# Performance work log

Measured on AMD Instinct MI355X. Metric: run time of the kernel, lower is better.

Reference implementation:

```python
import jax, jax.numpy as jnp
import numpy as np

B, G, C, Hmlp, R = 4, 2048, 384, 1536, 96
NH = 6          # attention heads
V = 6           # number of 2D views (len(out_transform_2d))
NC = 1024       # number of clusters for segment_csr
GX = GY = 32    # grid shape per view
SCALE_FACTOR = 0.5  # args.scale_factor
COEF_PRO = 0.5      # args.coef_pro
EPS_LN = 1e-5
EPS_BN = 1e-5


def _forward(x, center1, norm1_g, norm1_b, qkv_w, proj_w, proj_b, norm2_g, norm2_b,
             fc1_w, fc1_b, fc2_w, fc2_b, ada1_w, ada1_b, ada2_w, ada2_b,
             bn3_g, bn3_b, bn3_m, bn3_v, bn2_g, bn2_b, bn2_m, bn2_v,
             norm3_g, norm3_b, a1_qkv_w, a1_proj_w, a1_proj_b,
             mask, idx_ptr, sorted_cluster_indices, cluster, flat_grid_index,
             grid_shape_x, grid_shape_y):
    B_, G1, C_ = x.shape
    hd = C_ // NH

    def ln(t, g, b):
        mu = t.mean(-1, keepdims=True)
        var = ((t - mu) ** 2).mean(-1, keepdims=True)
        return (t - mu) * jax.lax.rsqrt(var + EPS_LN) * g + b

    def bn_gelu(t, g, b, m, v):  # BatchNorm1d (eval) + GELU
        t = (t - m) * jax.lax.rsqrt(v + EPS_BN) * g + b
        return jax.nn.gelu(t, approximate=False)

    # ---- multi-head self-attention sublayer ----
    h = ln(x, norm1_g, norm1_b)
    qkv = (h @ qkv_w).reshape(B_, G1, 3, NH, hd).transpose(2, 0, 3, 1, 4)
    q, k, v = qkv[0], qkv[1], qkv[2]
    attn = jax.nn.softmax(jnp.einsum('bhqd,bhkd->bhqk', q, k) * hd ** -0.5, axis=-1)
    o = jnp.einsum('bhqk,bhkd->bhqd', attn, v).transpose(0, 2, 1, 3).reshape(B_, G1, C_)
    x = x + o @ proj_w + proj_b

    # ---- MLP + adapter sublayer ----
    h2 = ln(x, norm2_g, norm2_b)
    ffn = jax.nn.gelu(h2 @ fc1_w + fc1_b, approximate=False) @ fc2_w + fc2_b
    a = ffn @ ada1_w + ada1_b
    a = a * jax.nn.sigmoid(1.702 * a)      # QuickGELU
    ada = a @ ada2_w + ada2_b
    x = x + ffn + SCALE_FACTOR * ada

    cls_x = x[:, :1]
    pts = x[:, 1:]
    Gp = G1 - 1
    N = B_ * Gp

    # ---- 3D branch: segment_csr max/mean over clusters, gather back ----
    feat = pts.reshape(N, C_)
    fs = feat[sorted_cluster_indices]
    seg = cluster[sorted_cluster_indices]          # sorted segment ids (CSR order)
    nc = idx_ptr.shape[0] - 1
    cnt = jax.ops.segment_sum(jnp.ones((N,), feat.dtype), seg, nc)
    fsum = jax.ops.segment_sum(fs, seg, nc)
    fmax = jax.ops.segment_max(fs, seg, nc)
    fmax = jnp.where(cnt[:, None] > 0, fmax, 0.0)
    fmean = fsum / jnp.maximum(cnt, 1.0)[:, None]
    x3d = bn_gelu(fmax + fmean, bn3_g, bn3_b, bn3_m, bn3_v)[cluster].reshape(pts.shape)

    # ---- per-view 2D branch: masked attn + scatter_max/mean over grid cells ----
    dim_size = center1.shape[0] * grid_shape_x * grid_shape_y
    nviews = center1.shape[1]
    views = []
    for i in range(nviews):
        fx = pts.reshape(N, C_)
        h3 = ln(fx, norm3_g[i], norm3_b[i]).reshape(B_, Gp, C_)
        qkv1 = (h3 @ a1_qkv_w[i]).reshape(B_, Gp, 3, C_).transpose(2, 0, 1, 3)
        q1, k1, v1 = qkv1[0], qkv1[1], qkv1[2]
        s = jnp.einsum('bqd,bkd->bqk', q1, k1) * C_ ** -0.5
        s = jnp.where(mask[i][None], s, jnp.finfo(s.dtype).min)
        o1 = jnp.einsum('bqk,bkd->bqd', jax.nn.softmax(s, axis=-1), v1) @ a1_proj_w[i] + a1_proj_b[i]
        fx = o1.reshape(N, C_) + fx
        gi = flat_grid_index[i]
        gc = jax.ops.segment_sum(jnp.ones((N,), fx.dtype), gi, dim_size)
        gs = jax.ops.segment_sum(fx, gi, dim_size)
        gm = jax.ops.segment_max(fx, gi, dim_size)
        gm = jnp.where(gc[:, None] > 0, gm, 0.0)
        cell = bn_gelu(gs / jnp.maximum(gc, 1.0)[:, None] + gm,
                       bn2_g[i], bn2_b[i], bn2_m[i], bn2_v[i])
        views.append(cell[gi].reshape(pts.shape))

    # ---- cosine-similarity weighted fusion across views ----
    x_sup = jnp.stack(views, 0)                     # [V,B,G,C]
    dot = jnp.sum(x_sup * x3d[None], -1)
    nrm = jnp.linalg.norm(x_sup, axis=-1) * jnp.linalg.norm(x3d, axis=-1)[None]
    sims = (dot / jnp.maximum(nrm, 1e-8) + 1.0) / 2.0
    sims = sims / sims.sum(0, keepdims=True)
    x_sup_w = jnp.sum(x_sup * sims[..., None], 0)
    pts = pts + COEF_PRO * x_sup_w
    return jnp.concatenate([cls_x, pts], axis=1)


def setup_inputs() -> dict:
    rng = np.random.default_rng(0)
    key = jax.random.key(0)
    N = B * G
    # consistent cluster structure: every cluster non-empty
    cluster = np.concatenate([np.arange(NC), rng.integers(0, NC, N - NC)]).astype(np.int32)
    rng.shuffle(cluster)
    sorted_idx = np.argsort(cluster, kind='stable').astype(np.int32)
    counts = np.bincount(cluster, minlength=NC)
    idx_ptr = np.concatenate([[0], np.cumsum(counts)]).astype(np.int32)
    flat_grid_index = rng.integers(0, B * GX * GY, (V, N)).astype(np.int32)
    mask = (rng.random((V, G, G)) < 0.25) | np.eye(G, dtype=bool)[None]
    ks = jax.random.split(key, 16)
    f32 = jnp.float32
    def w(k, shape, s=0.02):
        return jax.random.normal(k, shape, f32) * s
    return {
        'x': jax.random.normal(ks[0], (B, G + 1, C), f32),
        'center1': jax.random.normal(ks[1], (B, V, G, 3), f32),
        'norm1_g': jnp.ones((C,), f32), 'norm1_b': jnp.zeros((C,), f32),
        'qkv_w': w(ks[2], (C, 3 * C)), 'proj_w': w(ks[3], (C, C)), 'proj_b': jnp.zeros((C,), f32),
        'norm2_g': jnp.ones((C,), f32), 'norm2_b': jnp.zeros((C,), f32),
        'fc1_w': w(ks[4], (C, Hmlp)), 'fc1_b': jnp.zeros((Hmlp,), f32),
        'fc2_w': w(ks[5], (Hmlp, C)), 'fc2_b': jnp.zeros((C,), f32),
        'ada1_w': w(ks[6], (C, R)), 'ada1_b': jnp.zeros((R,), f32),
        'ada2_w': w(ks[7], (R, C)), 'ada2_b': jnp.zeros((C,), f32),
        'bn3_g': jnp.ones((C,), f32), 'bn3_b': jnp.zeros((C,), f32),
        'bn3_m': w(ks[8], (C,), 0.1), 'bn3_v': jnp.ones((C,), f32) + jax.random.uniform(ks[9], (C,), f32) * 0.5,
        'bn2_g': jnp.ones((V, C), f32), 'bn2_b': jnp.zeros((V, C), f32),
        'bn2_m': w(ks[10], (V, C), 0.1), 'bn2_v': jnp.ones((V, C), f32) + jax.random.uniform(ks[11], (V, C), f32) * 0.5,
        'norm3_g': jnp.ones((V, C), f32), 'norm3_b': jnp.zeros((V, C), f32),
        'a1_qkv_w': w(ks[12], (V, C, 3 * C)), 'a1_proj_w': w(ks[13], (V, C, C)), 'a1_proj_b': jnp.zeros((V, C), f32),
        'mask': jnp.asarray(mask),
        'idx_ptr': jnp.asarray(idx_ptr),
        'sorted_cluster_indices': jnp.asarray(sorted_idx),
        'cluster': jnp.asarray(cluster),
        'flat_grid_index': jnp.asarray(flat_grid_index),
        'grid_shape_x': GX,
        'grid_shape_y': GY,
    }


def reference(x, center1, norm1_g, norm1_b, qkv_w, proj_w, proj_b, norm2_g, norm2_b,
              fc1_w, fc1_b, fc2_w, fc2_b, ada1_w, ada1_b, ada2_w, ada2_b,
              bn3_g, bn3_b, bn3_m, bn3_v, bn2_g, bn2_b, bn2_m, bn2_v,
              norm3_g, norm3_b, a1_qkv_w, a1_proj_w, a1_proj_b,
              mask, idx_ptr, sorted_cluster_indices, cluster, flat_grid_index,
              grid_shape_x, grid_shape_y):
    return _forward(x, center1, norm1_g, norm1_b, qkv_w, proj_w, proj_b, norm2_g, norm2_b,
                    fc1_w, fc1_b, fc2_w, fc2_b, ada1_w, ada1_b, ada2_w, ada2_b,
                    bn3_g, bn3_b, bn3_m, bn3_v, bn2_g, bn2_b, bn2_m, bn2_v,
                    norm3_g, norm3_b, a1_qkv_w, a1_proj_w, a1_proj_b,
                    mask, idx_ptr, sorted_cluster_indices, cluster, flat_grid_index,
                    grid_shape_x, grid_shape_y)
```

## Files before the change

kernel.cpp:

```cpp
#include <hip/hip_runtime.h>
#include <math.h>

typedef short bf16x8 __attribute__((ext_vector_type(8)));
typedef float f32x4 __attribute__((ext_vector_type(4)));

#define GLL16(g, l) \
  __builtin_amdgcn_global_load_lds((__attribute__((address_space(1))) const unsigned int*)(g), \
                                   (__attribute__((address_space(3))) unsigned int*)(l), 16, 0, 0)

__device__ __forceinline__ float wsum(float v){
  #pragma unroll
  for (int o=32;o;o>>=1) v += __shfl_xor(v,o);
  return v;
}
__device__ __forceinline__ float geluf(float x){
  return 0.5f*x*(1.0f+erff(x*0.7071067811865475f));
}
__device__ __forceinline__ short fbf(float f){
  unsigned u = __float_as_uint(f);
  unsigned r = (u + 0x7fffu + ((u>>16)&1u)) >> 16;
  return (short)r;
}
__device__ __forceinline__ float bff(short s){
  return __uint_as_float(((unsigned)(unsigned short)s)<<16);
}
__device__ __forceinline__ unsigned fkey(float f){
  unsigned b=__float_as_uint(f);
  return (b&0x80000000u)? ~b : (b|0x80000000u);
}
__device__ __forceinline__ float fdec(unsigned k){
  unsigned b=(k&0x80000000u)? (k&0x7fffffffu) : ~k;
  return __uint_as_float(b);
}

__global__ void detect_mask_kernel(const int* __restrict__ m, long long n, int* flag){
  long long i = (long long)blockIdx.x*256 + threadIdx.x;
  bool bad = (i<n) && (m[i]!=0 && m[i]!=1);
  if (__any(bad)) { if ((threadIdx.x&63)==0) atomicOr(flag,1); }
}
__global__ void mask_bits_kernel(const void* __restrict__ m, unsigned long long* __restrict__ mb,
                                 long long nOut, const int* __restrict__ flag){
  long long i = (long long)blockIdx.x*256 + threadIdx.x;
  if (i>=nOut) return;
  int mode = *flag;
  unsigned long long bits = 0;
  if (mode){
    const unsigned long long* p = (const unsigned long long*)((const unsigned char*)m + i*64);
    #pragma unroll
    for (int k=0;k<8;k++){
      unsigned long long v = p[k];
      #pragma unroll
      for (int b=0;b<8;b++)
        bits |= (unsigned long long)(((v>>(b*8))&0xffull)!=0) << (k*8+b);
    }
  } else {
    const int4* p = (const int4*)((const int*)m + i*64);
    #pragma unroll
    for (int k=0;k<16;k++){
      int4 v = p[k];
      bits |= (unsigned long long)(v.x!=0) << (k*4+0);
      bits |= (unsigned long long)(v.y!=0) << (k*4+1);
      bits |= (unsigned long long)(v.z!=0) << (k*4+2);
      bits |= (unsigned long long)(v.w!=0) << (k*4+3);
    }
  }
  mb[i] = bits;
}

__device__ __forceinline__ float epi(float v, const float* bias, int col, int act){
  if (bias) v += bias[col];
  if (act==1) v = geluf(v);
  else if (act==2) v = v*(1.f/(1.f+__expf(-1.702f*v)));
  return v;
}

#define XBM 128
#define XBN 128
#define XBK 32
__global__ __launch_bounds__(256)
void gemm_bf16_big(const short* __restrict__ A, int lda, long long sA,
                   const short* __restrict__ B, int ldb, long long sB,
                   const float* __restrict__ bias, long long sBias,
                   const float* __restrict__ res, int ldr, long long sR,
                   void* __restrict__ out, int ldo, long long sO, int outbf16,
                   int M, int N, int K, int act, int KS)
{
  __shared__ short As[XBM*XBK];
  __shared__ short Bs[XBN*XBK];
  int zz = blockIdx.z;
  int z = zz / KS, ks = zz - z*KS;
  A += (long long)z*sA; B += (long long)z*sB;
  if (res) res += (long long)z*sR;
  if (bias) bias += (long long)z*sBias;
  float* outF = (float*)out + (long long)z*sO;
  short* outH = (short*)out + (long long)z*sO;

  int tid = threadIdx.x;
  int rowBase = blockIdx.y*XBM;
  int colBase = blockIdx.x*XBN;

  int Kc = ((K + KS*XBK - 1)/(KS*XBK))*XBK;
  int kbeg = ks*Kc;
  int kend = min(K, kbeg+Kc);
  if (kbeg >= kend) return;

  int w = tid>>6;
  int lane = tid&63;
  int lm = lane&15, quad = lane>>4;
  int waveM = w>>1, waveN = w&1;

  int arow0 = min(rowBase + w*32 + lm,      M-1);
  int arow1 = min(rowBase + w*32 + 16 + lm, M-1);
  int brow0 = min(colBase + w*32 + lm,      N-1);
  int brow1 = min(colBase + w*32 + 16 + lm, N-1);
  const short* Ag0 = A + (long long)arow0*lda + quad*8;
  const short* Ag1 = A + (long long)arow1*lda + quad*8;
  const short* Bg0 = B + (long long)brow0*ldb + quad*8;
  const short* Bg1 = B + (long long)brow1*ldb + quad*8;
  short* Al0 = &As[(w*2+0)*512];
  short* Al1 = &As[(w*2+1)*512];
  short* Bl0 = &Bs[(w*2+0)*512];
  short* Bl1 = &Bs[(w*2+1)*512];

  f32x4 acc[4][4] = {};

  for (int k0=kbeg; k0<kend; k0+=XBK){
    GLL16(Ag0 + k0, Al0);
    GLL16(Ag1 + k0, Al1);
    GLL16(Bg0 + k0, Bl0);
    GLL16(Bg1 + k0, Bl1);
    __syncthreads();
    bf16x8 af[4], bfr[4];
    #pragma unroll
    for (int tm=0;tm<4;tm++) af[tm]  = *(bf16x8*)&As[(waveM*4+tm)*512 + quad*128 + lm*8];
    #pragma unroll
    for (int tn=0;tn<4;tn++) bfr[tn] = *(bf16x8*)&Bs[(waveN*4+tn)*512 + quad*128 + lm*8];
    #pragma unroll
    for (int tm=0;tm<4;tm++)
      #pragma unroll
      for (int tn=0;tn<4;tn++)
        acc[tm][tn] = __builtin_amdgcn_mfma_f32_16x16x32_bf16(af[tm], bfr[tn], acc[tm][tn], 0,0,0);
    __syncthreads();
  }

  #pragma unroll
  for (int tm=0;tm<4;tm++){
    #pragma unroll
    for (int tn=0;tn<4;tn++){
      int col = colBase + waveN*64 + tn*16 + lm;
      if (col>=N) continue;
      #pragma unroll
      for (int reg=0;reg<4;reg++){
        int row = rowBase + waveM*64 + tm*16 + quad*4 + reg;
        if (row>=M) continue;
        float v = acc[tm][tn][reg];
        if (KS>1){ atomicAdd(&outF[(long long)row*ldo+col], v); continue; }
        v = epi(v, bias, col, act);
        if (res) v += res[(long long)row*ldr+col];
        if (outbf16) outH[(long long)row*ldo+col] = fbf(v);
        else         outF[(long long)row*ldo+col] = v;
      }
    }
  }
}

__global__ __launch_bounds__(256)
void gemm_bf16_s(const short* __restrict__ A, int lda, long long sA,
                 const short* __restrict__ B, int ldb, long long sB,
                 const float* __restrict__ bias, long long sBias,
                 const float* __restrict__ res, int ldr, long long sR,
                 void* __restrict__ out, int ldo, long long sO, int outbf16,
                 int M, int N, int K, int act)
{
  __shared__ short As[64*32];
  __shared__ short Bs[64*32];
  int z = blockIdx.z;
  A += (long long)z*sA; B += (long long)z*sB;
  if (res) res += (long long)z*sR;
  if (bias) bias += (long long)z*sBias;
  float* outF = (float*)out + (long long)z*sO;
  short* outH = (short*)out + (long long)z*sO;

  int tid = threadIdx.x;
  int rowBase = blockIdx.y*64;
  int colBase = blockIdx.x*64;

  int w = tid>>6;
  int lane = tid&63;
  int lm = lane&15, quad = lane>>4;
  int wm = w>>1, wn = w&1;

  int arow = min(rowBase + w*16 + lm, M-1);
  int brow = min(colBase + w*16 + lm, N-1);
  const short* Ag = A + (long long)arow*lda + quad*8;
  const short* Bg = B + (long long)brow*ldb + quad*8;
  short* Al = &As[w*512];
  short* Bl = &Bs[w*512];

  f32x4 acc[2][2] = {};

  for (int k0=0; k0<K; k0+=32){
    GLL16(Ag + k0, Al);
    GLL16(Bg + k0, Bl);
    __syncthreads();
    bf16x8 af[2], bfr[2];
    #pragma unroll
    for (int tm=0;tm<2;tm++) af[tm]  = *(bf16x8*)&As[(wm*2+tm)*512 + quad*128 + lm*8];
    #pragma unroll
    for (int tn=0;tn<2;tn++) bfr[tn] = *(bf16x8*)&Bs[(wn*2+tn)*512 + quad*128 + lm*8];
    #pragma unroll
    for (int tm=0;tm<2;tm++)
      #pragma unroll
      for (int tn=0;tn<2;tn++)
        acc[tm][tn] = __builtin_amdgcn_mfma_f32_16x16x32_bf16(af[tm], bfr[tn], acc[tm][tn], 0,0,0);
    __syncthreads();
  }

  #pragma unroll
  for (int tm=0;tm<2;tm++){
    #pragma unroll
    for (int tn=0;tn<2;tn++){
      int col = colBase + wn*32 + tn*16 + lm;
      if (col>=N) continue;
      #pragma unroll
      for (int reg=0;reg<4;reg++){
        int row = rowBase + wm*32 + tm*16 + quad*4 + reg;
        if (row>=M) continue;
        float v = epi(acc[tm][tn][reg], bias, col, act);
        if (res) v += res[(long long)row*ldr+col];
        if (outbf16==2){
          int bb = row>>11;
          outH[((long long)bb*384 + col)*2048 + (row&2047)] = fbf(v);
        }
        else if (outbf16) outH[(long long)row*ldo+col] = fbf(v);
        else              outF[(long long)row*ldo+col] = v;
      }
    }
  }
}

__global__ __launch_bounds__(256,2)
void flash_view(const short* __restrict__ QK6, const short* __restrict__ Vt6,
                const unsigned long long* __restrict__ maskbits, short* __restrict__ O6)
{
  __shared__ char lds[58112];
  const float scale = 0.05103103630798288f;
  int id = blockIdx.x;
  int xcd = id & 7;
  int j = id >> 3;
  int vb = xcd*3 + (j>>5);
  int qt = j & 31;
  int v = vb >> 2, b = vb & 3;
  int tid=threadIdx.x, w=tid>>6, lane=tid&63, lm=lane&15, quad=lane>>4;

  const short* Qp = QK6 + ((long long)v*8192 + b*2048 + qt*64)*768;
  const short* Kp = QK6 + ((long long)v*8192 + b*2048)*768 + 384;
  const short* Vp = Vt6 + (long long)(v*4+b)*384*2048;
  const unsigned long long* Mb = maskbits + (long long)v*2048*32 + (long long)qt*64*32;
  short* Op = O6 + ((long long)v*8192 + b*2048 + qt*64)*384;

  short* P = (short*)(lds + 49152);
  float* alphaL = (float*)(lds + 57856);

  bf16x8 af[12];
  #pragma unroll
  for (int c=0;c<12;c++)
    af[c] = *(const bf16x8*)(Qp + (long long)(w*16+lm)*768 + c*32 + quad*8);

  float m_i[4], l_i[4];
  #pragma unroll
  for (int r=0;r<4;r++){ m_i[r]=-3.0e38f; l_i[r]=0.f; }
  f32x4 Oacc[4][6] = {};

  for (int kt=0; kt<32; kt++){
    #pragma unroll
    for (int c=0;c<12;c++)
      GLL16(Kp + (long long)(kt*64 + w*16 + lm)*768 + c*32 + quad*8, (short*)(lds + w*12288 + c*1024));
    __syncthreads();
    unsigned long long mb[4];
    #pragma unroll
    for (int r=0;r<4;r++)
      mb[r] = Mb[(long long)(w*16+quad*4+r)*32 + kt];
    f32x4 S[4];
    #pragma unroll
    for (int i=0;i<4;i++) S[i] = (f32x4){0.f,0.f,0.f,0.f};
    __builtin_amdgcn_s_setprio(1);
    #pragma unroll
    for (int kc=0;kc<12;kc++){
      #pragma unroll
      for (int ct=0;ct<4;ct++){
        bf16x8 bf = *(bf16x8*)(lds + ct*12288 + kc*1024 + quad*256 + lm*16);
        S[ct] = __builtin_amdgcn_mfma_f32_16x16x32_bf16(af[kc], bf, S[ct], 0,0,0);
      }
    }
    __builtin_amdgcn_s_setprio(0);
    #pragma unroll
    for (int r=0;r<4;r++){
      unsigned long long t = mb[r] >> lm;
      S[0][r] = ((unsigned)t      & 1u) ? S[0][r]*scale : -3.0e38f;
      S[1][r] = ((unsigned)(t>>16)& 1u) ? S[1][r]*scale : -3.0e38f;
      S[2][r] = ((unsigned)(t>>32)& 1u) ? S[2][r]*scale : -3.0e38f;
      S[3][r] = ((unsigned)(t>>48)& 1u) ? S[3][r]*scale : -3.0e38f;
    }
    float alpha[4], mnew[4];
    #pragma unroll
    for (int r=0;r<4;r++){
      float rm = S[0][r];
      #pragma unroll
      for (int ct=1;ct<4;ct++) rm = fmaxf(rm, S[ct][r]);
      #pragma unroll
      for (int o=1;o<16;o<<=1) rm = fmaxf(rm, __shfl_xor(rm, o));
      mnew[r] = fmaxf(m_i[r], rm);
      alpha[r] = __expf(m_i[r]-mnew[r]);
      m_i[r] = mnew[r];
    }
    float rs[4] = {0.f,0.f,0.f,0.f};
    #pragma unroll
    for (int ct=0;ct<4;ct++){
      #pragma unroll
      for (int r=0;r<4;r++){
        float sv = S[ct][r];
        float p = (sv > -1.0e37f) ? __expf(sv - mnew[r]) : 0.f;
        rs[r] += p;
        P[(w*16+quad*4+r)*68 + ct*16 + lm] = fbf(p);
      }
    }
    #pragma unroll
    for (int r=0;r<4;r++){
      #pragma unroll
      for (int o=1;o<16;o<<=1) rs[r] += __shfl_xor(rs[r], o);
      l_i[r] = l_i[r]*alpha[r] + rs[r];
    }
    if (lm==0){
      #pragma unroll
      for (int r=0;r<4;r++) alphaL[w*16+quad*4+r] = alpha[r];
    }
    bf16x8 Vreg[6][2];
    #pragma unroll
    for (int jj=0;jj<6;jj++)
      #pragma unroll
      for (int kk=0;kk<2;kk++)
        Vreg[jj][kk] = *(const bf16x8*)(Vp + (long long)((w*6+jj)*16+lm)*2048 + kt*64 + kk*32 + quad*8);
    __syncthreads();
    f32x4 am[4];
    #pragma unroll
    for (int m=0;m<4;m++) am[m] = *(f32x4*)&alphaL[m*16 + quad*4];
    #pragma unroll
    for (int m=0;m<4;m++)
      #pragma unroll
      for (int tn=0;tn<6;tn++)
        Oacc[m][tn] *= am[m];
    __builtin_amdgcn_s_setprio(1);
    #pragma unroll
    for (int kk=0;kk<2;kk++){
      bf16x8 ap[4];
      #pragma unroll
      for (int m=0;m<4;m++) ap[m] = *(bf16x8*)&P[(m*16+lm)*68 + kk*32 + quad*8];
      #pragma unroll
      for (int tn=0;tn<6;tn++){
        #pragma unroll
        for (int m=0;m<4;m++)
          Oacc[m][tn] = __builtin_amdgcn_mfma_f32_16x16x32_bf16(ap[m], Vreg[tn][kk], Oacc[m][tn], 0,0,0);
      }
    }
    __builtin_amdgcn_s_setprio(0);
  }

  __syncthreads();
  if (lm==0){
    #pragma unroll
    for (int r=0;r<4;r++) alphaL[w*16+quad*4+r] = l_i[r];
  }
  __syncthreads();
  f32x4 lv[4];
  #pragma unroll
  for (int m=0;m<4;m++) lv[m] = *(f32x4*)&alphaL[m*16 + quad*4];
  #pragma unroll
  for (int m=0;m<4;m++){
    #pragma unroll
    for (int tn=0;tn<6;tn++){
      #pragma unroll
      for (int reg=0;reg<4;reg++){
        Op[(long long)(m*16+quad*4+reg)*384 + (w*6+tn)*16 + lm] = fbf(Oacc[m][tn][reg] / lv[m][reg]);
      }
    }
  }
}

__global__ __launch_bounds__(256,4)
void flash_inner(const short* __restrict__ QKV, const short* __restrict__ Vt,
                 short* __restrict__ O)
{
  __shared__ char lds[17152];
  int id = blockIdx.x;
  int xcd = id & 7;
  int j = id >> 3;
  int bh = xcd*3 + j/33;
  int qt = j%33;
  int b=bh/6, h=bh-b*6;
  int tid=threadIdx.x, w=tid>>6, lane=tid&63, lm=lane&15, quad=lane>>4;

  const short* Qb = QKV + (long long)b*2049*1152 + h*64;
  const short* Kb = Qb + 384;
  const short* Vtp = Vt + (long long)bh*64*2112;
  short* Op = O + ((long long)b*2049 + qt*64)*384 + h*64;

  short* P = (short*)(lds + 8192);
  float* alphaL = (float*)(lds + 16896);

  int qr = min(qt*64 + w*16 + lm, 2048);
  bf16x8 af[2];
  #pragma unroll
  for (int c=0;c<2;c++)
    af[c] = *(const bf16x8*)(Qb + (long long)qr*1152 + c*32 + quad*8);

  float m_i[4], l_i[4];
  #pragma unroll
  for (int r=0;r<4;r++){ m_i[r]=-3.0e38f; l_i[r]=0.f; }
  f32x4 Oacc[4] = {};

  {
    int kr0 = min(w*16 + lm, 2048);
    #pragma unroll
    for (int c=0;c<2;c++)
      GLL16(Kb + (long long)kr0*1152 + c*32 + quad*8, (short*)(lds + w*2048 + c*1024));
  }

  for (int kt=0; kt<33; kt++){
    __syncthreads();
    f32x4 S[4];
    #pragma unroll
    for (int i=0;i<4;i++) S[i] = (f32x4){0.f,0.f,0.f,0.f};
    __builtin_amdgcn_s_setprio(1);
    #pragma unroll
    for (int kc=0;kc<2;kc++){
      #pragma unroll
      for (int ct=0;ct<4;ct++){
        bf16x8 bf = *(bf16x8*)(lds + ct*2048 + kc*1024 + quad*256 + lm*16);
        S[ct] = __builtin_amdgcn_mfma_f32_16x16x32_bf16(af[kc], bf, S[ct], 0,0,0);
      }
    }
    __builtin_amdgcn_s_setprio(0);
    #pragma unroll
    for (int ct=0;ct<4;ct++){
      int scol = kt*64 + ct*16 + lm;
      bool ok = scol <= 2048;
      #pragma unroll
      for (int r=0;r<4;r++) S[ct][r] = ok ? S[ct][r]*0.125f : -3.0e38f;
    }
    float alpha[4], mnew[4];
    #pragma unroll
    for (int r=0;r<4;r++){
      float rm = S[0][r];
      #pragma unroll
      for (int ct=1;ct<4;ct++) rm = fmaxf(rm, S[ct][r]);
      #pragma unroll
      for (int o=1;o<16;o<<=1) rm = fmaxf(rm, __shfl_xor(rm, o));
      mnew[r] = fmaxf(m_i[r], rm);
      alpha[r] = __expf(m_i[r]-mnew[r]);
      m_i[r] = mnew[r];
    }
    float rs[4] = {0.f,0.f,0.f,0.f};
    #pragma unroll
    for (int ct=0;ct<4;ct++){
      #pragma unroll
      for (int r=0;r<4;r++){
        float sv = S[ct][r];
        float p = (sv > -1.0e37f) ? __expf(sv - mnew[r]) : 0.f;
        rs[r] += p;
        P[(w*16+quad*4+r)*68 + ct*16 + lm] = fbf(p);
      }
    }
    #pragma unroll
    for (int r=0;r<4;r++){
      #pragma unroll
      for (int o=1;o<16;o<<=1) rs[r] += __shfl_xor(rs[r], o);
      l_i[r] = l_i[r]*alpha[r] + rs[r];
    }
    if (lm==0){
      #pragma unroll
      for (int r=0;r<4;r++) alphaL[w*16+quad*4+r] = alpha[r];
    }
    bf16x8 Vreg[2];
    #pragma unroll
    for (int kk=0;kk<2;kk++)
      Vreg[kk] = *(const bf16x8*)(Vtp + (long long)(w*16+lm)*2112 + kt*64 + kk*32 + quad*8);
    __syncthreads();
    if (kt < 32){
      int krn = min((kt+1)*64 + w*16 + lm, 2048);
      #pragma unroll
      for (int c=0;c<2;c++)
        GLL16(Kb + (long long)krn*1152 + c*32 + quad*8, (short*)(lds + w*2048 + c*1024));
    }
    f32x4 am[4];
    #pragma unroll
    for (int m=0;m<4;m++) am[m] = *(f32x4*)&alphaL[m*16 + quad*4];
    #pragma unroll
    for (int m=0;m<4;m++) Oacc[m] *= am[m];
    __builtin_amdgcn_s_setprio(1);
    #pragma unroll
    for (int kk=0;kk<2;kk++){
      bf16x8 ap[4];
      #pragma unroll
      for (int m=0;m<4;m++) ap[m] = *(bf16x8*)&P[(m*16+lm)*68 + kk*32 + quad*8];
      #pragma unroll
      for (int m=0;m<4;m++)
        Oacc[m] = __builtin_amdgcn_mfma_f32_16x16x32_bf16(ap[m], Vreg[kk], Oacc[m], 0,0,0);
    }
    __builtin_amdgcn_s_setprio(0);
  }

  __syncthreads();
  if (lm==0){
    #pragma unroll
    for (int r=0;r<4;r++) alphaL[w*16+quad*4+r] = l_i[r];
  }
  __syncthreads();
  f32x4 lv[4];
  #pragma unroll
  for (int m=0;m<4;m++) lv[m] = *(f32x4*)&alphaL[m*16 + quad*4];
  #pragma unroll
  for (int m=0;m<4;m++){
    #pragma unroll
    for (int reg=0;reg<4;reg++){
      int row = qt*64 + m*16 + quad*4 + reg;
      if (row < 2049)
        Op[(long long)(m*16+quad*4+reg)*384 + w*16 + lm] = fbf(Oacc[m][reg] / lv[m][reg]);
    }
  }
}

__global__ __launch_bounds__(128)
void ln_bf16_kernel(const float* __restrict__ in, const float* __restrict__ g,
                    const float* __restrict__ bt, short* __restrict__ out)
{
  long long row = blockIdx.x;
  const float* p = in + row*384;
  int tid = threadIdx.x;
  float v0=p[tid], v1=p[tid+128], v2=p[tid+256];
  float s = v0+v1+v2;
  float ss = v0*v0+v1*v1+v2*v2;
  __shared__ float r1[2], r2[2];
  s = wsum(s); ss = wsum(ss);
  int wid=tid>>6, lane=tid&63;
  if (lane==0){ r1[wid]=s; r2[wid]=ss; }
  __syncthreads();
  float mean=(r1[0]+r1[1])*(1.f/384.f);
  float var =(r2[0]+r2[1])*(1.f/384.f)-mean*mean;
  float rstd=rsqrtf(var+1e-5f);
  short* o = out + row*384;
  o[tid]     = fbf((v0-mean)*rstd*g[tid]+bt[tid]);
  o[tid+128] = fbf((v1-mean)*rstd*g[tid+128]+bt[tid+128]);
  o[tid+256] = fbf((v2-mean)*rstd*g[tid+256]+bt[tid+256]);
}

__global__ __launch_bounds__(128)
void ln6_kernel(const float* __restrict__ in, const float* __restrict__ g6,
                const float* __restrict__ b6, short* __restrict__ out6)
{
  long long row = blockIdx.x;
  const float* p = in + row*384;
  int tid = threadIdx.x;
  float v0=p[tid], v1=p[tid+128], v2=p[tid+256];
  float s = v0+v1+v2;
  float ss = v0*v0+v1*v1+v2*v2;
  __shared__ float r1[2], r2[2];
  s = wsum(s); ss = wsum(ss);
  int wid=tid>>6, lane=tid&63;
  if (lane==0){ r1[wid]=s; r2[wid]=ss; }
  __syncthreads();
  float mean=(r1[0]+r1[1])*(1.f/384.f);
  float var =(r2[0]+r2[1])*(1.f/384.f)-mean*mean;
  float rstd=rsqrtf(var+1e-5f);
  float n0=(v0-mean)*rstd, n1=(v1-mean)*rstd, n2=(v2-mean)*rstd;
  #pragma unroll
  for (int i=0;i<6;i++){
    const float* g = g6 + i*384;
    const float* bt = b6 + i*384;
    short* o = out6 + (long long)i*8192*384 + row*384;
    o[tid]     = fbf(n0*g[tid]+bt[tid]);
    o[tid+128] = fbf(n1*g[tid+128]+bt[tid+128]);
    o[tid+256] = fbf(n2*g[tid+256]+bt[tid+256]);
  }
}

__global__ void cvt_kernel(const float* __restrict__ in, short* __restrict__ out, long long n4){
  long long i = (long long)blockIdx.x*256 + threadIdx.x;
  if (i<n4){
    float4 f = ((const float4*)in)[i];
    short4 s;
    s.x=fbf(f.x); s.y=fbf(f.y); s.z=fbf(f.z); s.w=fbf(f.w);
    ((short4*)out)[i]=s;
  }
}

__global__ __launch_bounds__(256)
void tconv_kernel(const float* __restrict__ in, int ldin, long long sIn, long long sIn2, int zmod,
                  int R, int C, short* __restrict__ out, int ldout, long long sOut)
{
  __shared__ float tile[32][33];
  int z = blockIdx.z;
  const float* ip = in + (long long)(z/zmod)*sIn + (long long)(z%zmod)*sIn2;
  short* op = out + (long long)z*sOut;
  int r0 = blockIdx.x*32;
  int c0 = blockIdx.y*32;
  int tx = threadIdx.x&31, ty = threadIdx.x>>5;
  #pragma unroll
  for (int i=0;i<4;i++){
    int r = r0 + ty + i*8, c = c0 + tx;
    tile[ty+i*8][tx] = (r<R && c<C) ? ip[(long long)r*ldin + c] : 0.f;
  }
  __syncthreads();
  #pragma unroll
  for (int i=0;i<4;i++){
    int oc = c0 + ty + i*8;
    int orr = r0 + tx;
    if (oc<C && orr<ldout) op[(long long)oc*ldout + orr] = fbf(tile[tx][ty+i*8]);
  }
}

__global__ __launch_bounds__(256)
void tconv16_kernel(const short* __restrict__ in, int ldin, long long sIn, long long sIn2, int zmod,
                    int R, int C, short* __restrict__ out, int ldout, long long sOut)
{
  __shared__ short tile[32][34];
  int z = blockIdx.z;
  const short* ip = in + (long long)(z/zmod)*sIn + (long long)(z%zmod)*sIn2;
  short* op = out + (long long)z*sOut;
  int r0 = blockIdx.x*32;
  int c0 = blockIdx.y*32;
  int tx = threadIdx.x&31, ty = threadIdx.x>>5;
  #pragma unroll
  for (int i=0;i<4;i++){
    int r = r0 + ty + i*8, c = c0 + tx;
    tile[ty+i*8][tx] = (r<R && c<C) ? ip[(long long)r*ldin + c] : (short)0;
  }
  __syncthreads();
  #pragma unroll
  for (int i=0;i<4;i++){
    int oc = c0 + ty + i*8;
    int orr = r0 + tx;
    if (oc<C && orr<ldout) op[(long long)oc*ldout + orr] = tile[tx][ty+i*8];
  }
}

__global__ void ew_x2_kernel(float* x1, const float* ffn, const float* ada, long long n){
  long long i=(long long)blockIdx.x*256+threadIdx.x;
  if (i<n) x1[i] = x1[i] + ffn[i] + 0.5f*ada[i];
}
__global__ void copy_pts_kernel(const float* __restrict__ x2, float* __restrict__ pts){
  long long i=(long long)blockIdx.x*256+threadIdx.x;
  if (i < 8192ll*384){
    long long b = i/(2048ll*384);
    long long rem = i%(2048ll*384);
    pts[i] = x2[(b*2049+1)*384 + rem];
  }
}
__global__ void copy_cls_kernel(const float* __restrict__ x2, float* __restrict__ out){
  int i = blockIdx.x*256+threadIdx.x;
  if (i < 4*384){
    int b=i/384, c=i%384;
    out[(long long)b*2049*384 + c] = x2[(long long)b*2049*384 + c];
  }
}

__global__ __launch_bounds__(128)
void scatter_seg_kernel(const float* __restrict__ feat, const int* __restrict__ seg,
                        float* __restrict__ fsum, unsigned* __restrict__ fmax,
                        float* __restrict__ cnt,
                        long long zFeat, long long zSeg, long long zSum, long long zCnt)
{
  int n = blockIdx.x, z = blockIdx.y;
  feat += (long long)z*zFeat; seg += (long long)z*zSeg;
  fsum += (long long)z*zSum; fmax += (long long)z*zSum; cnt += (long long)z*zCnt;
  int s = seg[n];
  const float* p = feat + (long long)n*384;
  int tid = threadIdx.x;
  #pragma unroll
  for (int k=0;k<3;k++){
    int c = tid + k*128;
    float v = p[c];
    atomicAdd(&fsum[(long long)s*384+c], v);
    atomicMax(&fmax[(long long)s*384+c], fkey(v));
  }
  if (tid==0) atomicAdd(&cnt[s], 1.0f);
}

__global__ __launch_bounds__(128)
void cell_kernel(const float* __restrict__ fsum, const unsigned* __restrict__ fmax,
                 const float* __restrict__ cnt,
                 const float* __restrict__ g, const float* __restrict__ bb,
                 const float* __restrict__ m, const float* __restrict__ v,
                 float* __restrict__ out, long long zSum, long long zCnt, long long zP)
{
  int s = blockIdx.x, z = blockIdx.y;
  fsum += (long long)z*zSum; fmax += (long long)z*zSum; cnt += (long long)z*zCnt;
  g += (long long)z*zP; bb += (long long)z*zP; m += (long long)z*zP; v += (long long)z*zP;
  out += (long long)z*zSum;
  float cn = cnt[s];
  float denom = fmaxf(cn, 1.f);
  int tid = threadIdx.x;
  #pragma unroll
  for (int k=0;k<3;k++){
    int c = tid + k*128;
    float mx = (cn>0.f) ? fdec(fmax[(long long)s*384+c]) : 0.f;
    float t = mx + fsum[(long long)s*384+c]/denom;
    t = (t - m[c])*rsqrtf(v[c]+1e-5f)*g[c] + bb[c];
    out[(long long)s*384+c] = geluf(t);
  }
}

__global__ __launch_bounds__(128)
void combine_kernel(const float* __restrict__ pts, const float* __restrict__ cell3,
                    const int* __restrict__ cluster, const float* __restrict__ cell2,
                    const int* __restrict__ gidx, float* __restrict__ out)
{
  int n = blockIdx.x;
  int tid = threadIdx.x;
  __shared__ float sdot[6], ssq[6], sw[6];
  __shared__ int soff[6];
  __shared__ float red[2][2];
  __shared__ float sn3;
  const float* x3 = cell3 + (long long)cluster[n]*384;
  int wid=tid>>6, lane=tid&63;
  float sq=0.f;
  for (int c=tid;c<384;c+=128){ float v=x3[c]; sq+=v*v; }
  sq = wsum(sq);
  if (lane==0) red[0][wid]=sq;
  __syncthreads();
  if (tid==0) sn3 = sqrtf(red[0][0]+red[0][1]);
  __syncthreads();
  for (int i=0;i<6;i++){
    int gi = gidx[(long long)i*8192 + n];
    if (tid==0) soff[i]=gi;
    const float* r = cell2 + ((long long)i*4096 + gi)*384;
    float d=0.f, s2=0.f;
    for (int c=tid;c<384;c+=128){ float a=r[c]; d+=a*x3[c]; s2+=a*a; }
    d = wsum(d); s2 = wsum(s2);
    if (lane==0){ red[0][wid]=d; red[1][wid]=s2; }
    __syncthreads();
    if (tid==0){ sdot[i]=red[0][0]+red[0][1]; ssq[i]=red[1][0]+red[1][1]; }
    __syncthreads();
  }
  if (tid==0){
    float ssumv=0.f; float sims[6];
    for (int i=0;i<6;i++){
      float nrm = sqrtf(ssq[i])*sn3;
      float s = (sdot[i]/fmaxf(nrm,1e-8f) + 1.f)*0.5f;
      sims[i]=s; ssumv+=s;
    }
    for (int i=0;i<6;i++) sw[i]=sims[i]/ssumv;
  }
  __syncthreads();
  int b = n>>11, gp = n&2047;
  float* o = out + ((long long)(b*2049 + 1 + gp))*384;
  for (int c=tid;c<384;c+=128){
    float acc=0.f;
    #pragma unroll
    for (int i=0;i<6;i++){
      const float* r = cell2 + ((long long)i*4096 + soff[i])*384;
      acc += sw[i]*r[c];
    }
    o[c] = pts[(long long)n*384+c] + 0.5f*acc;
  }
}

static inline void launch_gemm16b(hipStream_t s, const short* A,int lda,long long sA,
  const short* B,int ldb,long long sB, const float* bias, long long sBias,
  const float* res,int ldr,long long sR, void* out,int ldo,long long sO,int outbf16,
  int M,int N,int K,int act,int nz,int KS)
{
  dim3 g((N+XBN-1)/XBN,(M+XBM-1)/XBM,(unsigned)(nz*KS));
  hipLaunchKernelGGL(gemm_bf16_big,g,dim3(256),0,s,
    A,lda,sA,B,ldb,sB,bias,sBias,res,ldr,sR,out,ldo,sO,outbf16,M,N,K,act,KS);
}
static inline void launch_gemm16s(hipStream_t s, const short* A,int lda,long long sA,
  const short* B,int ldb,long long sB, const float* bias, long long sBias,
  const float* res,int ldr,long long sR, void* out,int ldo,long long sO,int outbf16,
  int M,int N,int K,int act,int nz)
{
  dim3 g((N+63)/64,(M+63)/64,(unsigned)nz);
  hipLaunchKernelGGL(gemm_bf16_s,g,dim3(256),0,s,
    A,lda,sA,B,ldb,sB,bias,sBias,res,ldr,sR,out,ldo,sO,outbf16,M,N,K,act);
}
static inline void launch_tconv(hipStream_t s, const float* in,int ldin,long long sIn,long long sIn2,int zmod,
  int R,int C, short* out,int ldout,long long sOut,int nz)
{
  dim3 g((ldout+31)/32,(C+31)/32,(unsigned)nz);
  hipLaunchKernelGGL(tconv_kernel,g,dim3(256),0,s, in,ldin,sIn,sIn2,zmod,R,C,out,ldout,sOut);
}
static inline void launch_tconv16(hipStream_t s, const short* in,int ldin,long long sIn,long long sIn2,int zmod,
  int R,int C, short* out,int ldout,long long sOut,int nz)
{
  dim3 g((ldout+31)/32,(C+31)/32,(unsigned)nz);
  hipLaunchKernelGGL(tconv16_kernel,g,dim3(256),0,s, in,ldin,sIn,sIn2,zmod,R,C,out,ldout,sOut);
}
static inline void launch_cvt(hipStream_t s, const float* in, short* out, long long n){
  long long n4 = n/4;
  hipLaunchKernelGGL(cvt_kernel,dim3((unsigned)((n4+255)/256)),dim3(256),0,s,in,out,n4);
}

extern "C" void kernel_launch(void* const* d_in, const int* in_sizes, int n_in,
                              void* d_out, int out_size, void* d_ws, size_t ws_size,
                              hipStream_t stream)
{
  const float* x       = (const float*)d_in[0];
  const float* norm1_g = (const float*)d_in[2];
  const float* norm1_b = (const float*)d_in[3];
  const float* qkv_w   = (const float*)d_in[4];
  const float* proj_w  = (const float*)d_in[5];
  const float* proj_b  = (const float*)d_in[6];
  const float* norm2_g = (const float*)d_in[7];
  const float* norm2_b = (const float*)d_in[8];
  const float* fc1_w   = (const float*)d_in[9];
  const float* fc1_b   = (const float*)d_in[10];
  const float* fc2_w   = (const float*)d_in[11];
  const float* fc2_b   = (const float*)d_in[12];
  const float* ada1_w  = (const float*)d_in[13];
  const float* ada1_b  = (const float*)d_in[14];
  const float* ada2_w  = (const float*)d_in[15];
  const float* ada2_b  = (const float*)d_in[16];
  const float* bn3_g   = (const float*)d_in[17];
  const float* bn3_b   = (const float*)d_in[18];
  const float* bn3_m   = (const float*)d_in[19];
  const float* bn3_v   = (const float*)d_in[20];
  const float* bn2_g   = (const float*)d_in[21];
  const float* bn2_b   = (const float*)d_in[22];
  const float* bn2_m   = (const float*)d_in[23];
  const float* bn2_v   = (const float*)d_in[24];
  const float* norm3_g = (const float*)d_in[25];
  const float* norm3_b = (const float*)d_in[26];
  const float* a1_qkv_w  = (const float*)d_in[27];
  const float* a1_proj_w = (const float*)d_in[28];
  const float* a1_proj_b = (const float*)d_in[29];
  const void*  maskp     = d_in[30];
  const int*   cluster   = (const int*)d_in[33];
  const int*   fgi       = (const int*)d_in[34];
  float* out = (float*)d_out;

  size_t off = 0;
  char* wsb = (char*)d_ws;
  auto alloc = [&](size_t bytes)->void*{
    void* p = wsb + off;
    off += (bytes + 255) & ~(size_t)255;
    return p;
  };
  short*    bufHh = (short*)alloc(8196ll*384*2);
  float*    ptsb  = (float*)alloc(8192ll*384*4);
  float*    cnt   = (float*)alloc(1024*4);
  float*    fsum  = (float*)alloc(1024ll*384*4);
  unsigned* fmaxe = (unsigned*)alloc(1024ll*384*4);
  float*    cell3 = (float*)alloc(1024ll*384*4);
  unsigned char* maskb = (unsigned char*)alloc(6ll*2048*2048);
  float*    gc6   = (float*)alloc(6ll*4096*4);
  short*    qkvT  = (short*)alloc(1152ll*384*2);
  short*    projT = (short*)alloc(384ll*384*2);
  short*    fc1T  = (short*)alloc(1536ll*384*2);
  short*    fc2T  = (short*)alloc(384ll*1536*2);
  short*    ada1T = (short*)alloc(96ll*384*2);
  short*    ada2T = (short*)alloc(384ll*96*2);
  short*    a1qkvT  = (short*)alloc(6ll*1152*384*2);
  short*    a1projT = (short*)alloc(6ll*384*384*2);
  int*      flag  = (int*)alloc(256);
  char* arena = (char*)alloc(188743680);
  char* A0 = arena;
  char* A1 = arena + 75497472;
  char* A2 = arena + 150994944;
  short* bufQh = (short*)(A0 + 0);
  float* bufO  = (float*)(A0 + 20971520);
  short* bufOh = (short*)(A0 + 35651584);
  short* bufAh = (short*)(A0 + 44040192);
  float* bufX  = (float*)(A0 + 46137344);
  float* bufAda= (float*)(A0 + 0);
  short* Vt_i  = (short*)(A1 + 0);
  short* bufTh = (short*)(A1 + 8388608);
  short* QK6   = (short*)(A0 + 0);
  short* Vt6   = (short*)(A1 + 0);
  short* O6    = (short*)(A2 + 0);
  short* bufHh6= (short*)(A2 + 0);
  float* bufT6 = (float*)(A0 + 0);
  float* gsum6 = (float*)(A1 + 0);
  unsigned* gmaxe6 = (unsigned*)(A1 + 37748736);
  float* cell2 = (float*)(A0 + 0);

  unsigned long long* maskbits = (unsigned long long*)maskb;

  hipMemsetAsync(flag, 0, 4, stream);
  {
    long long nInt = 6ll*2048*2048/4;
    detect_mask_kernel<<<dim3((unsigned)((nInt+255)/256)),dim3(256),0,stream>>>((const int*)maskp, nInt, flag);
    long long nOut = 6ll*2048*32;
    mask_bits_kernel<<<dim3((unsigned)((nOut+255)/256)),dim3(256),0,stream>>>(maskp, maskbits, nOut, flag);
  }

  launch_tconv(stream, qkv_w, 1152, 0,0,1, 384,1152, qkvT, 384, 0, 1);
  launch_tconv(stream, proj_w, 384, 0,0,1, 384,384,  projT, 384, 0, 1);
  launch_tconv(stream, fc1_w, 1536, 0,0,1, 384,1536, fc1T, 384, 0, 1);
  launch_tconv(stream, fc2_w, 384,  0,0,1, 1536,384, fc2T, 1536, 0, 1);
  launch_tconv(stream, ada1_w, 96,  0,0,1, 384,96,   ada1T, 384, 0, 1);
  launch_tconv(stream, ada2_w, 384, 0,0,1, 96,384,   ada2T, 96, 0, 1);
  launch_tconv(stream, a1_qkv_w, 1152, 384ll*1152,0,1, 384,1152, a1qkvT, 384, 1152ll*384, 6);
  launch_tconv(stream, a1_proj_w, 384, 384ll*384,0,1, 384,384,  a1projT, 384, 384ll*384, 6);

  ln_bf16_kernel<<<8196,128,0,stream>>>(x, norm1_g, norm1_b, bufHh);
  launch_gemm16b(stream, bufHh,384,0, qkvT,384,0, nullptr,0, nullptr,0,0,
                 bufQh,1152,0,1, 8196,1152,384, 0, 1,1);
  launch_tconv16(stream, bufQh + 768, 1152, 2049ll*1152, 64, 6, 2049, 64, Vt_i, 2112, 64ll*2112, 24);
  flash_inner<<<dim3(792),256,0,stream>>>(bufQh, Vt_i, bufOh);
  launch_gemm16s(stream, bufOh,384,0, projT,384,0, proj_b,0, x,384,0,
                 bufX,384,0,0, 8196,384,384, 0, 1);
  ln_bf16_kernel<<<8196,128,0,stream>>>(bufX, norm2_g, norm2_b, bufHh);
  launch_gemm16b(stream, bufHh,384,0, fc1T,384,0, fc1_b,0, nullptr,0,0,
                 bufTh,1536,0,1, 8196,1536,384, 1, 1,1);
  launch_gemm16s(stream, bufTh,1536,0, fc2T,1536,0, fc2_b,0, nullptr,0,0,
                 bufO,384,0,0, 8196,384,1536, 0, 1);
  launch_cvt(stream, bufO, bufOh, 8196ll*384);
  launch_gemm16s(stream, bufOh,384,0, ada1T,384,0, ada1_b,0, nullptr,0,0,
                 bufAh,96,0,1, 8196,96,384, 2, 1);
  launch_gemm16s(stream, bufAh,96,0, ada2T,96,0, ada2_b,0, nullptr,0,0,
                 bufAda,384,0,0, 8196,384,96, 0, 1);
  ew_x2_kernel<<<dim3((8196*384+255)/256),256,0,stream>>>(bufX, bufO, bufAda, 8196ll*384);
  copy_cls_kernel<<<6,256,0,stream>>>(bufX, out);
  copy_pts_kernel<<<dim3((8192*384+255)/256),256,0,stream>>>(bufX, ptsb);

  hipMemsetAsync(cnt, 0, 1024*4, stream);
  hipMemsetAsync(fsum, 0, 1024ll*384*4, stream);
  hipMemsetAsync(fmaxe, 0, 1024ll*384*4, stream);
  scatter_seg_kernel<<<dim3(8192,1),128,0,stream>>>(ptsb, cluster, fsum, fmaxe, cnt, 0,0,0,0);
  cell_kernel<<<dim3(1024,1),128,0,stream>>>(fsum, fmaxe, cnt, bn3_g,bn3_b,bn3_m,bn3_v, cell3, 0,0,0);

  ln6_kernel<<<8192,128,0,stream>>>(ptsb, norm3_g, norm3_b, bufHh6);
  launch_gemm16b(stream, bufHh6,384,8192ll*384, a1qkvT,384,1152ll*384,
                 nullptr,0, nullptr,0,0, QK6,768,8192ll*768,1, 8192,768,384, 0, 6,1);
  launch_gemm16s(stream, bufHh6,384,8192ll*384, a1qkvT + 768ll*384,384,1152ll*384,
                 nullptr,0, nullptr,0,0, Vt6,2048,4ll*384*2048,2, 8192,384,384, 0, 6);

  flash_view<<<dim3(768),256,0,stream>>>(QK6, Vt6, maskbits, O6);

  launch_gemm16s(stream, O6,384,8192ll*384, a1projT,384,384ll*384,
                 a1_proj_b,384, ptsb,384,0,
                 bufT6,384,8192ll*384,0, 8192,384,384, 0, 6);
  hipMemsetAsync(gc6, 0, 6ll*4096*4, stream);
  hipMemsetAsync(gsum6, 0, 6ll*4096*384*4, stream);
  hipMemsetAsync(gmaxe6, 0, 6ll*4096*384*4, stream);
  scatter_seg_kernel<<<dim3(8192,6),128,0,stream>>>(bufT6, fgi, gsum6, gmaxe6, gc6,
      8192ll*384, 8192, 4096ll*384, 4096);
  cell_kernel<<<dim3(4096,6),128,0,stream>>>(gsum6, gmaxe6, gc6,
      bn2_g, bn2_b, bn2_m, bn2_v, cell2, 4096ll*384, 4096, 384);

  combine_kernel<<<8192,128,0,stream>>>(ptsb, cell3, cluster, cell2, fgi, out);
}
```

Measured before the change: 1.546 ms.

## Fuse residual add with cls/pts split, widen combine kernel, use big GEMM tiles

Three changes. First, the residual add and the two copy kernels (cls token and point rows) are merged into one elementwise kernel that writes straight into the output and the pts buffer, saving two launches and a full read/write pass. Second, combine_kernel now runs 384 threads per block, one wavefront per view, so the six dot products and norms are computed in parallel with a single barrier. Third, several N=384 GEMMs (proj, fc2, view proj) move from the small-tile kernel to the big-tile kernel, which may cut the number of blocks and lower occupancy.

```diff
diff --git a/kernel.cpp b/kernel.cpp
--- a/kernel.cpp
+++ b/kernel.cpp
@@ -644,24 +644,16 @@
   }
 }
 
-__global__ void ew_x2_kernel(float* x1, const float* ffn, const float* ada, long long n){
+__global__ void ew_fuse_kernel(const float* __restrict__ x1, const float* __restrict__ ffn,
+                               const float* __restrict__ ada,
+                               float* __restrict__ ptsb, float* __restrict__ out){
   long long i=(long long)blockIdx.x*256+threadIdx.x;
-  if (i<n) x1[i] = x1[i] + ffn[i] + 0.5f*ada[i];
-}
-__global__ void copy_pts_kernel(const float* __restrict__ x2, float* __restrict__ pts){
-  long long i=(long long)blockIdx.x*256+threadIdx.x;
-  if (i < 8192ll*384){
-    long long b = i/(2048ll*384);
-    long long rem = i%(2048ll*384);
-    pts[i] = x2[(b*2049+1)*384 + rem];
-  }
-}
-__global__ void copy_cls_kernel(const float* __restrict__ x2, float* __restrict__ out){
-  int i = blockIdx.x*256+threadIdx.x;
-  if (i < 4*384){
-    int b=i/384, c=i%384;
-    out[(long long)b*2049*384 + c] = x2[(long long)b*2049*384 + c];
-  }
+  if (i >= 8196ll*384) return;
+  float v = x1[i] + ffn[i] + 0.5f*ada[i];
+  long long row = i/384; int c = (int)(i - row*384);
+  long long b = row/2049; long long g = row - b*2049;
+  if (g == 0) out[b*2049*384 + c] = v;
+  else        ptsb[((b*2048) + (g-1))*384 + c] = v;
 }
 
 __global__ __launch_bounds__(128)
@@ -710,59 +702,46 @@
   }
 }
 
-__global__ __launch_bounds__(128)
+__global__ __launch_bounds__(384)
 void combine_kernel(const float* __restrict__ pts, const float* __restrict__ cell3,
                     const int* __restrict__ cluster, const float* __restrict__ cell2,
                     const int* __restrict__ gidx, float* __restrict__ out)
 {
   int n = blockIdx.x;
   int tid = threadIdx.x;
-  __shared__ float sdot[6], ssq[6], sw[6];
+  int w = tid>>6, lane = tid&63;
+  __shared__ float sdot[6], ssq[6], sn3s;
   __shared__ int soff[6];
-  __shared__ float red[2][2];
-  __shared__ float sn3;
   const float* x3 = cell3 + (long long)cluster[n]*384;
-  int wid=tid>>6, lane=tid&63;
-  float sq=0.f;
-  for (int c=tid;c<384;c+=128){ float v=x3[c]; sq+=v*v; }
-  sq = wsum(sq);
-  if (lane==0) red[0][wid]=sq;
+  int gi = gidx[(long long)w*8192 + n];
+  const float* r = cell2 + ((long long)w*4096 + gi)*384;
+  float d=0.f, s2=0.f, q3=0.f;
+  #pragma unroll
+  for (int k=0;k<6;k++){
+    int c = lane + k*64;
+    float a = r[c], x = x3[c];
+    d += a*x; s2 += a*a; q3 += x*x;
+  }
+  d = wsum(d); s2 = wsum(s2); q3 = wsum(q3);
+  if (lane==0){ sdot[w]=d; ssq[w]=s2; soff[w]=gi; if (w==0) sn3s=q3; }
   __syncthreads();
-  if (tid==0) sn3 = sqrtf(red[0][0]+red[0][1]);
-  __syncthreads();
+  float sn3 = sqrtf(sn3s);
+  float sims[6]; float ssumv=0.f;
+  #pragma unroll
   for (int i=0;i<6;i++){
-    int gi = gidx[(long long)i*8192 + n];
-    if (tid==0) soff[i]=gi;
-    const float* r = cell2 + ((long long)i*4096 + gi)*384;
-    float d=0.f, s2=0.f;
-    for (int c=tid;c<384;c+=128){ float a=r[c]; d+=a*x3[c]; s2+=a*a; }
-    d = wsum(d); s2 = wsum(s2);
-    if (lane==0){ red[0][wid]=d; red[1][wid]=s2; }
-    __syncthreads();
-    if (tid==0){ sdot[i]=red[0][0]+red[0][1]; ssq[i]=red[1][0]+red[1][1]; }
-    __syncthreads();
-  }
-  if (tid==0){
-    float ssumv=0.f; float sims[6];
-    for (int i=0;i<6;i++){
-      float nrm = sqrtf(ssq[i])*sn3;
-      float s = (sdot[i]/fmaxf(nrm,1e-8f) + 1.f)*0.5f;
-      sims[i]=s; ssumv+=s;
-    }
-    for (int i=0;i<6;i++) sw[i]=sims[i]/ssumv;
-  }
-  __syncthreads();
+    float nrm = sqrtf(ssq[i])*sn3;
+    float s = (sdot[i]/fmaxf(nrm,1e-8f) + 1.f)*0.5f;
+    sims[i]=s; ssumv+=s;
+  }
+  int c = tid;
+  float acc=0.f;
+  #pragma unroll
+  for (int i=0;i<6;i++){
+    const float* rr = cell2 + ((long long)i*4096 + soff[i])*384;
+    acc += (sims[i]/ssumv)*rr[c];
+  }
   int b = n>>11, gp = n&2047;
-  float* o = out + ((long long)(b*2049 + 1 + gp))*384;
-  for (int c=tid;c<384;c+=128){
-    float acc=0.f;
-    #pragma unroll
-    for (int i=0;i<6;i++){
-      const float* r = cell2 + ((long long)i*4096 + soff[i])*384;
-      acc += sw[i]*r[c];
-    }
-    o[c] = pts[(long long)n*384+c] + 0.5f*acc;
-  }
+  out[((long long)(b*2049 + 1 + gp))*384 + c] = pts[(long long)n*384+c] + 0.5f*acc;
 }
 
 static inline void launch_gemm16b(hipStream_t s, const short* A,int lda,long long sA,
@@ -907,21 +886,19 @@
                  bufQh,1152,0,1, 8196,1152,384, 0, 1,1);
   launch_tconv16(stream, bufQh + 768, 1152, 2049ll*1152, 64, 6, 2049, 64, Vt_i, 2112, 64ll*2112, 24);
   flash_inner<<<dim3(792),256,0,stream>>>(bufQh, Vt_i, bufOh);
-  launch_gemm16s(stream, bufOh,384,0, projT,384,0, proj_b,0, x,384,0,
-                 bufX,384,0,0, 8196,384,384, 0, 1);
+  launch_gemm16b(stream, bufOh,384,0, projT,384,0, proj_b,0, x,384,0,
+                 bufX,384,0,0, 8196,384,384, 0, 1,1);
   ln_bf16_kernel<<<8196,128,0,stream>>>(bufX, norm2_g, norm2_b, bufHh);
   launch_gemm16b(stream, bufHh,384,0, fc1T,384,0, fc1_b,0, nullptr,0,0,
                  bufTh,1536,0,1, 8196,1536,384, 1, 1,1);
-  launch_gemm16s(stream, bufTh,1536,0, fc2T,1536,0, fc2_b,0, nullptr,0,0,
-                 bufO,384,0,0, 8196,384,1536, 0, 1);
+  launch_gemm16b(stream, bufTh,1536,0, fc2T,1536,0, fc2_b,0, nullptr,0,0,
+                 bufO,384,0,0, 8196,384,1536, 0, 1,1);
   launch_cvt(stream, bufO, bufOh, 8196ll*384);
   launch_gemm16s(stream, bufOh,384,0, ada1T,384,0, ada1_b,0, nullptr,0,0,
                  bufAh,96,0,1, 8196,96,384, 2, 1);
   launch_gemm16s(stream, bufAh,96,0, ada2T,96,0, ada2_b,0, nullptr,0,0,
                  bufAda,384,0,0, 8196,384,96, 0, 1);
-  ew_x2_kernel<<<dim3((8196*384+255)/256),256,0,stream>>>(bufX, bufO, bufAda, 8196ll*384);
-  copy_cls_kernel<<<6,256,0,stream>>>(bufX, out);
-  copy_pts_kernel<<<dim3((8192*384+255)/256),256,0,stream>>>(bufX, ptsb);
+  ew_fuse_kernel<<<dim3((unsigned)((8196ll*384+255)/256)),256,0,stream>>>(bufX, bufO, bufAda, ptsb, out);
 
   hipMemsetAsync(cnt, 0, 1024*4, stream);
   hipMemsetAsync(fsum, 0, 1024ll*384*4, stream);
@@ -937,9 +914,9 @@
 
   flash_view<<<dim3(768),256,0,stream>>>(QK6, Vt6, maskbits, O6);
 
-  launch_gemm16s(stream, O6,384,8192ll*384, a1projT,384,384ll*384,
+  launch_gemm16b(stream, O6,384,8192ll*384, a1projT,384,384ll*384,
                  a1_proj_b,384, ptsb,384,0,
-                 bufT6,384,8192ll*384,0, 8192,384,384, 0, 6);
+                 bufT6,384,8192ll*384,0, 8192,384,384, 0, 6,1);
   hipMemsetAsync(gc6, 0, 6ll*4096*4, stream);
   hipMemsetAsync(gsum6, 0, 6ll*4096*384*4, stream);
   hipMemsetAsync(gmaxe6, 0, 6ll*4096*384*4, stream);
@@ -948,5 +925,5 @@
   cell_kernel<<<dim3(4096,6),128,0,stream>>>(gsum6, gmaxe6, gc6,
       bn2_g, bn2_b, bn2_m, bn2_v, cell2, 4096ll*384, 4096, 384);
 
-  combine_kernel<<<8192,128,0,stream>>>(ptsb, cell3, cluster, cell2, fgi, out);
-}
+  combine_kernel<<<8192,384,0,stream>>>(ptsb, cell3, cluster, cell2, fgi, out);
+}
```

Result: slower. 1.587 ms (+2.6%).
